# Kernel tuning notes

Measured on AMD Instinct MI355X. Metric: run time of the kernel, lower is better.

## Reference

```python
import jax, jax.numpy as jnp
import numpy as np

N, D_IN, D_OUT, K = 8192, 64, 128, 16


def setup_inputs() -> dict:
    key = jax.random.key(0)
    k1, k2, k3 = jax.random.split(key, 3)
    x = jax.random.normal(k1, (N, D_IN), dtype=jnp.float32)
    W1 = jax.random.normal(k2, (2 * D_IN, D_OUT), dtype=jnp.float32) * 0.05
    b1 = jnp.zeros((D_OUT,), dtype=jnp.float32)
    W2 = jax.random.normal(k3, (D_OUT, D_OUT), dtype=jnp.float32) * 0.05
    b2 = jnp.zeros((D_OUT,), dtype=jnp.float32)
    return {"x": x, "W1": W1, "b1": b1, "W2": W2, "b2": b2, "k": K}


def reference(x, W1, b1, W2, b2, k):
    # dynamic kNN graph (PyG knn(x, x, k) includes self as nearest neighbor)
    sq = jnp.sum(x * x, axis=-1)                      # [N]
    dist = sq[:, None] + sq[None, :] - 2.0 * (x @ x.T)  # [N, N] squared dists
    _, idx = jax.lax.top_k(-dist, k)                  # [N, k] nearest indices
    x_j = x[idx]                                      # [N, k, D_IN] gather
    x_i = jnp.broadcast_to(x[:, None, :], x_j.shape)  # [N, k, D_IN]
    e = jnp.concatenate([x_i, x_j - x_i], axis=-1)    # [N, k, 2*D_IN]
    h = jax.nn.relu(e @ W1 + b1) @ W2 + b2            # [N, k, D_OUT]
    return jnp.mean(h, axis=1)                        # mean aggregation -> [N, D_OUT]
```

## Files before the change

### kernel.cpp

```cpp
#include <hip/hip_runtime.h>

#define N 8192
#define DIN 64
#define DOUT 128
#define KNN 16
#define MSAMP 2048
#define NBX 8
#define CAND_R 64
#define CAND_C (NBX * CAND_R)
#define EPS 1.0f
#define DELTA_Q 64
#define VCAP 128
#define ROWS_PRE 16

typedef unsigned long long u64;
typedef __attribute__((ext_vector_type(8))) short bf16x8;
typedef __attribute__((ext_vector_type(4))) float floatx4;

__device__ __forceinline__ unsigned mono(float f) {
    unsigned u = __float_as_uint(f);
    return (u & 0x80000000u) ? ~u : (u | 0x80000000u);
}
__device__ __forceinline__ unsigned short f2bf(float f) {
    unsigned u = __float_as_uint(f);
    return (unsigned short)((u + 0x7FFFu + ((u >> 16) & 1u)) >> 16);
}
__device__ __forceinline__ unsigned qdist(float dist) {
    int q = (int)(dist * 128.0f) + 2;
    q = max(q, 0); return (unsigned)min(q, 65535);
}

__global__ __launch_bounds__(256) void k_pre(const float* __restrict__ x,
                                             const float* __restrict__ W1,
                                             const float* __restrict__ b1,
                                             float* __restrict__ sq,
                                             float* __restrict__ sqs,
                                             unsigned short* __restrict__ Xh,
                                             float* __restrict__ U,
                                             float* __restrict__ V) {
    __shared__ float xs[ROWS_PRE][DIN];
    int t = threadIdx.x;
    int r0 = blockIdx.x * ROWS_PRE;
    float4 xv = ((const float4*)x)[(size_t)r0 * (DIN / 4) + t];
    ((float4*)xs)[t] = xv;
    ushort4 h4;
    h4.x = f2bf(xv.x); h4.y = f2bf(xv.y);
    h4.z = f2bf(xv.z); h4.w = f2bf(xv.w);
    *(ushort4*)&Xh[r0 * DIN + t * 4] = h4;
    __syncthreads();
    if (t < ROWS_PRE) {
        const float4* xr = (const float4*)xs[t];
        float s0 = 0.f, s1 = 0.f, s2 = 0.f, s3 = 0.f;
#pragma unroll
        for (int q = 0; q < DIN / 4; ++q) {
            float4 a = xr[q];
            s0 = fmaf(a.x, a.x, s0); s1 = fmaf(a.y, a.y, s1);
            s2 = fmaf(a.z, a.z, s2); s3 = fmaf(a.w, a.w, s3);
        }
        float sv = (s0 + s1) + (s2 + s3);
        sq[r0 + t] = sv;
        if ((t & 3) == 0) sqs[(r0 + t) >> 2] = sv;
    }
    int o = t & 127, g = t >> 7;
    float aU[8], aV[8];
#pragma unroll
    for (int u = 0; u < 8; ++u) { aU[u] = 0.f; aV[u] = 0.f; }
    for (int kk = 0; kk < DIN; ++kk) {
        float whi = W1[kk * DOUT + o];
        float wlo = W1[(DIN + kk) * DOUT + o];
        float wd = whi - wlo;
#pragma unroll
        for (int u = 0; u < 8; ++u) {
            float xvv = xs[g * 8 + u][kk];
            aU[u] = fmaf(xvv, wd, aU[u]);
            aV[u] = fmaf(xvv, wlo, aV[u]);
        }
    }
    float bb = b1[o];
#pragma unroll
    for (int u = 0; u < 8; ++u) {
        int r = r0 + g * 8 + u;
        U[(size_t)r * DOUT + o] = aU[u] + bb;
        V[(size_t)r * DOUT + o] = aV[u];
    }
}

__global__ __launch_bounds__(256, 4) void k_presample(const unsigned short* __restrict__ Xh,
                                                      const float* __restrict__ sq,
                                                      const float* __restrict__ sqs,
                                                      unsigned short* __restrict__ prekq) {
    __shared__ __align__(16) short ldsH[64 * 72];
    int tid = threadIdx.x, w = tid >> 6, l = tid & 63;
    int m = l & 15, ko = (l >> 4) * 8, quad = l >> 4;
    int bx = blockIdx.x;
    int rt = blockIdx.y * 4 + w;
    int irow = rt * 16 + m;
    size_t arow = (size_t)irow * DIN;
    bf16x8 iH0 = *(const bf16x8*)(Xh + arow + ko);
    bf16x8 iH1 = *(const bf16x8*)(Xh + arow + 32 + ko);
    float si = sq[irow];
    int srw = tid >> 3, scol8 = (tid & 7) * 8;
    for (int st = 0; st < 4; ++st) {
        int sbase = bx * 256 + st * 64;
        __syncthreads();
        *(bf16x8*)&ldsH[srw * 72 + scol8] =
            *(const bf16x8*)(Xh + (size_t)(4 * (sbase + srw)) * DIN + scol8);
        *(bf16x8*)&ldsH[(srw + 32) * 72 + scol8] =
            *(const bf16x8*)(Xh + (size_t)(4 * (sbase + srw + 32)) * DIN + scol8);
        __syncthreads();
#pragma unroll
        for (int it = 0; it < 4; ++it) {
            int br = it * 16 + m;
            bf16x8 sH0 = *(const bf16x8*)&ldsH[br * 72 + ko];
            bf16x8 sH1 = *(const bf16x8*)&ldsH[br * 72 + 32 + ko];
            floatx4 acc = {0.f, 0.f, 0.f, 0.f};
            acc = __builtin_amdgcn_mfma_f32_16x16x32_bf16(sH0, iH0, acc, 0, 0, 0);
            acc = __builtin_amdgcn_mfma_f32_16x16x32_bf16(sH1, iH1, acc, 0, 0, 0);
            int sc0 = sbase + it * 16 + quad * 4;
            float4 sj = *(const float4*)(sqs + sc0);
            u64 pk;
            {
                unsigned q0 = qdist(fmaf(-2.0f, acc[0], si + sj.x));
                unsigned q1 = qdist(fmaf(-2.0f, acc[1], si + sj.y));
                unsigned q2 = qdist(fmaf(-2.0f, acc[2], si + sj.z));
                unsigned q3 = qdist(fmaf(-2.0f, acc[3], si + sj.w));
                pk = (u64)q0 | ((u64)q1 << 16) | ((u64)q2 << 32) | ((u64)q3 << 48);
            }
            *(u64*)(prekq + (size_t)irow * MSAMP + sc0) = pk;
        }
    }
}

__global__ __launch_bounds__(256, 4) void k_tau(const unsigned short* __restrict__ prekq,
                                                float* __restrict__ tauf) {
    int w = threadIdx.x >> 6, l = threadIdx.x & 63;
    int row = blockIdx.x * 4 + w;
    unsigned v[MSAMP / 64];
#pragma unroll
    for (int u = 0; u < MSAMP / 64; ++u)
        v[u] = prekq[(size_t)row * MSAMP + l + 64 * u];
    unsigned p = 0;
#pragma unroll
    for (int b = 15; b >= 0; --b) {
        unsigned c16 = p | (1u << b);
        int cnt = 0;
#pragma unroll
        for (int u = 0; u < MSAMP / 64; ++u)
            cnt += __popcll(__ballot(v[u] < c16));
        if (cnt < 16) p = c16;
    }
    if (l == 0) tauf[row] = (float)p * (1.0f / 128.0f);
}

__global__ __launch_bounds__(256, 4) void k_main(const unsigned short* __restrict__ Xh,
                                                 const float* __restrict__ sq,
                                                 const float* __restrict__ tauf,
                                                 unsigned* __restrict__ cand,
                                                 unsigned* __restrict__ cntpart) {
    __shared__ __align__(16) short ldsH[64 * 72];
    int tid = threadIdx.x, w = tid >> 6, l = tid & 63;
    int m = l & 15, ko = (l >> 4) * 8;
    int bx = blockIdx.x;
    int rt = blockIdx.y * 4 + w;
    size_t arow = (size_t)(rt * 16 + m) * DIN;
    bf16x8 aH0 = *(const bf16x8*)(Xh + arow + ko);
    bf16x8 aH1 = *(const bf16x8*)(Xh + arow + 32 + ko);
    int rg[4]; float T[4]; float si[4]; int rowcnt[4];
#pragma unroll
    for (int reg = 0; reg < 4; ++reg) {
        rg[reg] = rt * 16 + (l >> 4) * 4 + reg;
        si[reg] = sq[rg[reg]];
        T[reg] = tauf[rg[reg]] + EPS - si[reg];
        rowcnt[reg] = 0;
    }
    int qs = l & 48;
    unsigned lmask = (1u << (l & 15)) - 1u;
    int srw = tid >> 3, scol8 = (tid & 7) * 8;

    for (int st = 0; st < 16; ++st) {
        int jbase = bx * 1024 + st * 64;
        __syncthreads();
        *(bf16x8*)&ldsH[srw * 72 + scol8] =
            *(const bf16x8*)(Xh + (size_t)(jbase + srw) * DIN + scol8);
        *(bf16x8*)&ldsH[(srw + 32) * 72 + scol8] =
            *(const bf16x8*)(Xh + (size_t)(jbase + srw + 32) * DIN + scol8);
        __syncthreads();
#pragma unroll
        for (int it = 0; it < 4; ++it) {
            int br = it * 16 + m;
            bf16x8 bH0 = *(const bf16x8*)&ldsH[br * 72 + ko];
            bf16x8 bH1 = *(const bf16x8*)&ldsH[br * 72 + 32 + ko];
            floatx4 acc = {0.f, 0.f, 0.f, 0.f};
            acc = __builtin_amdgcn_mfma_f32_16x16x32_bf16(aH0, bH0, acc, 0, 0, 0);
            acc = __builtin_amdgcn_mfma_f32_16x16x32_bf16(aH1, bH1, acc, 0, 0, 0);
            int jcol = jbase + it * 16 + m;
            float sqj = sq[jcol];
#pragma unroll
            for (int reg = 0; reg < 4; ++reg) {
                float tv = fmaf(-2.0f, acc[reg], sqj);
                bool pass = tv <= T[reg];
                u64 bal = __ballot(pass);
                if (bal) {
                    unsigned m16 = (unsigned)((bal >> qs) & 0xFFFFull);
                    if (pass) {
                        int slot = rowcnt[reg] + __popc(m16 & lmask);
                        if (slot < CAND_R)
                            cand[(size_t)rg[reg] * CAND_C + bx * CAND_R + slot] =
                                (qdist(tv + si[reg]) << 16) | (unsigned)jcol;
                    }
                    rowcnt[reg] += __popc(m16);
                }
            }
        }
    }
    if ((l & 15) == 0) {
#pragma unroll
        for (int reg = 0; reg < 4; ++reg)
            cntpart[rg[reg] * NBX + bx] = (unsigned)min(rowcnt[reg], CAND_R);
    }
}

__global__ __launch_bounds__(256) void k_exact(const float* __restrict__ x,
                                               const float* __restrict__ sq,
                                               const unsigned* __restrict__ cntpart,
                                               const unsigned* __restrict__ cand,
                                               int* __restrict__ knn) {
    __shared__ unsigned cj[4][CAND_C];
    __shared__ unsigned short vlist[4][VCAP];
    __shared__ u64 ekeys[4][VCAP];
    int w = threadIdx.x >> 6, l = threadIdx.x & 63;
    int row = blockIdx.x * 4 + w;
    int base = 0;
#pragma unroll
    for (int b = 0; b < NBX; ++b) {
        int c = (int)cntpart[row * NBX + b];
        c = min(c, CAND_R);
        if (l < c) cj[w][base + l] = cand[(size_t)row * CAND_C + b * CAND_R + l];
        base += c;
    }
    __syncthreads();
    unsigned kk[CAND_C / 64], qq[CAND_C / 64];
#pragma unroll
    for (int u = 0; u < CAND_C / 64; ++u) {
        int idx = l + 64 * u;
        kk[u] = (idx < base) ? cj[w][idx] : 0xFFFFFFFFu;
        qq[u] = (idx < base) ? (kk[u] >> 16) : 0xFFFFFFFFu;
    }
    unsigned p = 0;
#pragma unroll
    for (int b = 15; b >= 0; --b) {
        unsigned c16 = p | (1u << b);
        int cnt = 0;
#pragma unroll
        for (int u = 0; u < CAND_C / 64; ++u)
            cnt += __popcll(__ballot(qq[u] < c16));
        if (cnt < 16) p = c16;
    }
    unsigned thr = p + DELTA_Q;
    int nv = 0;
    u64 lm = (l == 63) ? 0xFFFFFFFFFFFFFFFFull >> 1 : (1ull << l) - 1ull;
#pragma unroll
    for (int u = 0; u < CAND_C / 64; ++u) {
        bool pred = qq[u] <= thr;
        u64 bal = __ballot(pred);
        int slot = nv + __popcll(bal & lm);
        if (pred && slot < VCAP) vlist[w][slot] = (unsigned short)(kk[u] & 0xFFFFu);
        nv += __popcll(bal);
    }
    nv = min(nv, VCAP);
    __syncthreads();
    float sqi = sq[row];
    const float* xi = x + (size_t)row * DIN;
#pragma unroll
    for (int r = 0; r < VCAP / 64; ++r) {
        int v = l + 64 * r;
        if (v < nv) {
            int j = (int)vlist[w][v];
            const float4* bj = (const float4*)(x + (size_t)j * DIN);
            float4 rb[16];
#pragma unroll
            for (int q = 0; q < DIN / 4; ++q) rb[q] = bj[q];
            float s0 = 0.f, s1 = 0.f, s2 = 0.f, s3 = 0.f;
#pragma unroll
            for (int q = 0; q < DIN / 4; ++q) {
                s0 = fmaf(xi[4 * q + 0], rb[q].x, s0);
                s1 = fmaf(xi[4 * q + 1], rb[q].y, s1);
                s2 = fmaf(xi[4 * q + 2], rb[q].z, s2);
                s3 = fmaf(xi[4 * q + 3], rb[q].w, s3);
            }
            float d = (s0 + s1) + (s2 + s3);
            float dist = fmaf(-2.0f, d, sqi + sq[j]);
            ekeys[w][v] = ((u64)mono(dist) << 32) | (unsigned)j;
        }
    }
#pragma unroll
    for (int r = 0; r < VCAP / 64; ++r) {
        int v = l + 64 * r;
        if (v < nv) {
            u64 mykey = ekeys[w][v];
            int rank = 0;
            for (int i = 0; i < nv; ++i)
                rank += (ekeys[w][i] < mykey) ? 1 : 0;
            if (rank < KNN)
                knn[row * KNN + rank] = (int)(unsigned)(mykey & 0xFFFFFFFFull);
        }
    }
}

__global__ __launch_bounds__(256) void k_aggout(const float* __restrict__ U,
                                                const float* __restrict__ V,
                                                const int* __restrict__ knn,
                                                const float* __restrict__ W2,
                                                const float* __restrict__ b2,
                                                float* __restrict__ out) {
    __shared__ float ag[8][DOUT];
    __shared__ float w2t[32 * DOUT];
    int t = threadIdx.x;
    int o = t & 127, g = t >> 7;
    int i0 = blockIdx.x * 8 + g * 4;
#pragma unroll
    for (int r = 0; r < 4; ++r) {
        int i = i0 + r;
        float u = U[(size_t)i * DOUT + o];
        const int* nb = knn + i * KNN;
        float acc = 0.f;
#pragma unroll
        for (int q = 0; q < KNN; ++q)
            acc += fmaxf(u + V[(size_t)nb[q] * DOUT + o], 0.0f);
        ag[g * 4 + r][o] = acc * (1.0f / KNN);
    }
    float a2[4] = {0.f, 0.f, 0.f, 0.f};
#pragma unroll
    for (int tile = 0; tile < 4; ++tile) {
        __syncthreads();
#pragma unroll
        for (int u = 0; u < 4; ++u)
            ((float4*)w2t)[t + u * 256] =
                ((const float4*)(W2 + tile * 32 * DOUT))[t + u * 256];
        __syncthreads();
#pragma unroll 8
        for (int kk = 0; kk < 32; ++kk) {
            float wv = w2t[kk * DOUT + o];
#pragma unroll
            for (int r = 0; r < 4; ++r)
                a2[r] = fmaf(ag[g * 4 + r][tile * 32 + kk], wv, a2[r]);
        }
    }
    float bb = b2[o];
#pragma unroll
    for (int r = 0; r < 4; ++r)
        out[(size_t)(i0 + r) * DOUT + o] = a2[r] + bb;
}

extern "C" void kernel_launch(void* const* d_in, const int* in_sizes, int n_in,
                              void* d_out, int out_size, void* d_ws, size_t ws_size,
                              hipStream_t stream) {
    const float* x  = (const float*)d_in[0];
    const float* W1 = (const float*)d_in[1];
    const float* b1 = (const float*)d_in[2];
    const float* W2 = (const float*)d_in[3];
    const float* b2 = (const float*)d_in[4];
    float* out = (float*)d_out;

    char* ws = (char*)d_ws;
    float*          sq      = (float*)(ws);
    float*          sqs     = (float*)(ws + 32768);
    float*          tauf    = (float*)(ws + 40960);
    int*            knn     = (int*)(ws + 73728);
    unsigned short* Xh      = (unsigned short*)(ws + 655360);
    unsigned*       cntpart = (unsigned*)(ws + 1703936);
    float*          U       = (float*)(ws + 2097152);
    float*          V       = (float*)(ws + 6291456);
    char*           region  = ws + 10485760;
    unsigned short* prekq   = (unsigned short*)region;
    unsigned*       cand    = (unsigned*)region;

    k_pre<<<N / ROWS_PRE, 256, 0, stream>>>(x, W1, b1, sq, sqs, Xh, U, V);
    k_presample<<<dim3(8, 128), 256, 0, stream>>>(Xh, sq, sqs, prekq);
    k_tau<<<N / 4, 256, 0, stream>>>(prekq, tauf);
    k_main<<<dim3(NBX, 128), 256, 0, stream>>>(Xh, sq, tauf, cand, cntpart);
    k_exact<<<N / 4, 256, 0, stream>>>(x, sq, cntpart, cand, knn);
    k_aggout<<<N / 8, 256, 0, stream>>>(U, V, knn, W2, b2, out);
}
```

Before: 183.6 us.

## Fuse sampled-distance and tau threshold kernels, keeping quantized distances in LDS

Combines the presample and tau kernels into a single kernel. Each 512-thread block computes the quantized distances from 16 rows to all 2048 samples with MFMA, stores them in a swizzled 64KB LDS buffer, then runs the bitwise radix threshold search straight from LDS. This removes the 32MB global write and read of prekq and one kernel launch. In exchange, sample rows are now read from global or L2 without LDS staging, and the 64KB of LDS per block limits occupancy.

```diff
diff --git a/kernel.cpp b/kernel.cpp
--- a/kernel.cpp
+++ b/kernel.cpp
@@ -85,71 +85,57 @@
     }
 }
 
-__global__ __launch_bounds__(256, 4) void k_presample(const unsigned short* __restrict__ Xh,
-                                                      const float* __restrict__ sq,
-                                                      const float* __restrict__ sqs,
-                                                      unsigned short* __restrict__ prekq) {
-    __shared__ __align__(16) short ldsH[64 * 72];
+__global__ __launch_bounds__(512, 4) void k_pretau(const unsigned short* __restrict__ Xh,
+                                                   const float* __restrict__ sq,
+                                                   const float* __restrict__ sqs,
+                                                   float* __restrict__ tauf) {
+    __shared__ __align__(16) unsigned short qls[16 * MSAMP];
     int tid = threadIdx.x, w = tid >> 6, l = tid & 63;
-    int m = l & 15, ko = (l >> 4) * 8, quad = l >> 4;
-    int bx = blockIdx.x;
-    int rt = blockIdx.y * 4 + w;
+    int m = l & 15, quad = l >> 4, ko = quad * 8;
+    int rt = blockIdx.x;
     int irow = rt * 16 + m;
     size_t arow = (size_t)irow * DIN;
     bf16x8 iH0 = *(const bf16x8*)(Xh + arow + ko);
     bf16x8 iH1 = *(const bf16x8*)(Xh + arow + 32 + ko);
     float si = sq[irow];
-    int srw = tid >> 3, scol8 = (tid & 7) * 8;
-    for (int st = 0; st < 4; ++st) {
-        int sbase = bx * 256 + st * 64;
-        __syncthreads();
-        *(bf16x8*)&ldsH[srw * 72 + scol8] =
-            *(const bf16x8*)(Xh + (size_t)(4 * (sbase + srw)) * DIN + scol8);
-        *(bf16x8*)&ldsH[(srw + 32) * 72 + scol8] =
-            *(const bf16x8*)(Xh + (size_t)(4 * (sbase + srw + 32)) * DIN + scol8);
-        __syncthreads();
-#pragma unroll
-        for (int it = 0; it < 4; ++it) {
-            int br = it * 16 + m;
-            bf16x8 sH0 = *(const bf16x8*)&ldsH[br * 72 + ko];
-            bf16x8 sH1 = *(const bf16x8*)&ldsH[br * 72 + 32 + ko];
-            floatx4 acc = {0.f, 0.f, 0.f, 0.f};
-            acc = __builtin_amdgcn_mfma_f32_16x16x32_bf16(sH0, iH0, acc, 0, 0, 0);
-            acc = __builtin_amdgcn_mfma_f32_16x16x32_bf16(sH1, iH1, acc, 0, 0, 0);
-            int sc0 = sbase + it * 16 + quad * 4;
-            float4 sj = *(const float4*)(sqs + sc0);
-            u64 pk;
-            {
-                unsigned q0 = qdist(fmaf(-2.0f, acc[0], si + sj.x));
-                unsigned q1 = qdist(fmaf(-2.0f, acc[1], si + sj.y));
-                unsigned q2 = qdist(fmaf(-2.0f, acc[2], si + sj.z));
-                unsigned q3 = qdist(fmaf(-2.0f, acc[3], si + sj.w));
-                pk = (u64)q0 | ((u64)q1 << 16) | ((u64)q2 << 32) | ((u64)q3 << 48);
-            }
-            *(u64*)(prekq + (size_t)irow * MSAMP + sc0) = pk;
-        }
-    }
-}
-
-__global__ __launch_bounds__(256, 4) void k_tau(const unsigned short* __restrict__ prekq,
-                                                float* __restrict__ tauf) {
-    int w = threadIdx.x >> 6, l = threadIdx.x & 63;
-    int row = blockIdx.x * 4 + w;
-    unsigned v[MSAMP / 64];
-#pragma unroll
-    for (int u = 0; u < MSAMP / 64; ++u)
-        v[u] = prekq[(size_t)row * MSAMP + l + 64 * u];
-    unsigned p = 0;
-#pragma unroll
-    for (int b = 15; b >= 0; --b) {
-        unsigned c16 = p | (1u << b);
-        int cnt = 0;
+    int swz = (m & 7) << 4;
+    for (int it = 0; it < 16; ++it) {
+        int s16 = w * 256 + it * 16;
+        size_t srowA = (size_t)(4 * (s16 + m)) * DIN;
+        bf16x8 sH0 = *(const bf16x8*)(Xh + srowA + ko);
+        bf16x8 sH1 = *(const bf16x8*)(Xh + srowA + 32 + ko);
+        floatx4 acc = {0.f, 0.f, 0.f, 0.f};
+        acc = __builtin_amdgcn_mfma_f32_16x16x32_bf16(sH0, iH0, acc, 0, 0, 0);
+        acc = __builtin_amdgcn_mfma_f32_16x16x32_bf16(sH1, iH1, acc, 0, 0, 0);
+        int sc0 = s16 + quad * 4;
+        float4 sj = *(const float4*)(sqs + sc0);
+        unsigned q0 = qdist(fmaf(-2.0f, acc[0], si + sj.x));
+        unsigned q1 = qdist(fmaf(-2.0f, acc[1], si + sj.y));
+        unsigned q2 = qdist(fmaf(-2.0f, acc[2], si + sj.z));
+        unsigned q3 = qdist(fmaf(-2.0f, acc[3], si + sj.w));
+        u64 pk = (u64)q0 | ((u64)q1 << 16) | ((u64)q2 << 32) | ((u64)q3 << 48);
+        *(u64*)&qls[m * MSAMP + (sc0 ^ swz)] = pk;
+    }
+    __syncthreads();
+#pragma unroll
+    for (int rr = 0; rr < 2; ++rr) {
+        int rsub = w * 2 + rr;
+        unsigned v[MSAMP / 64];
 #pragma unroll
         for (int u = 0; u < MSAMP / 64; ++u)
-            cnt += __popcll(__ballot(v[u] < c16));
-        if (cnt < 16) p = c16;
-    }
-    if (l == 0) tauf[row] = (float)p * (1.0f / 128.0f);
+            v[u] = qls[rsub * MSAMP + l + 64 * u];
+        unsigned p = 0;
+#pragma unroll
+        for (int b = 15; b >= 0; --b) {
+            unsigned c16 = p | (1u << b);
+            int cnt = 0;
+#pragma unroll
+            for (int u = 0; u < MSAMP / 64; ++u)
+                cnt += __popcll(__ballot(v[u] < c16));
+            if (cnt < 16) p = c16;
+        }
+        if (l == 0) tauf[rt * 16 + rsub] = (float)p * (1.0f / 128.0f);
+    }
 }
 
 __global__ __launch_bounds__(256, 4) void k_main(const unsigned short* __restrict__ Xh,
@@ -371,13 +357,10 @@
     unsigned*       cntpart = (unsigned*)(ws + 1703936);
     float*          U       = (float*)(ws + 2097152);
     float*          V       = (float*)(ws + 6291456);
-    char*           region  = ws + 10485760;
-    unsigned short* prekq   = (unsigned short*)region;
-    unsigned*       cand    = (unsigned*)region;
+    unsigned*       cand    = (unsigned*)(ws + 10485760);
 
     k_pre<<<N / ROWS_PRE, 256, 0, stream>>>(x, W1, b1, sq, sqs, Xh, U, V);
-    k_presample<<<dim3(8, 128), 256, 0, stream>>>(Xh, sq, sqs, prekq);
-    k_tau<<<N / 4, 256, 0, stream>>>(prekq, tauf);
+    k_pretau<<<N / 16, 512, 0, stream>>>(Xh, sq, sqs, tauf);
     k_main<<<dim3(NBX, 128), 256, 0, stream>>>(Xh, sq, tauf, cand, cntpart);
     k_exact<<<N / 4, 256, 0, stream>>>(x, sq, cntpart, cand, knn);
     k_aggout<<<N / 8, 256, 0, stream>>>(U, V, knn, W2, b2, out);
```

New measurement: 182.0 us. About the same (-0.9%).
